# Optimization experiments

Hardware: AMD Instinct MI355X
Metric: run time of the kernel (lower is better)

The kernel has to match this reference:

```python
import jax, jax.numpy as jnp
import numpy as np

S, B, D, H, HD = 2048, 4, 1280, 16, 80  # seq, batch, d_model, heads, head_dim
NSEG = 8


def setup_inputs() -> dict:
    key = jax.random.key(0)
    k0, k1, k2 = jax.random.split(key, 3)
    x = jax.random.normal(k0, (S, B, D), dtype=jnp.float32)
    Wqkv = jax.random.normal(k1, (D, 3 * D), dtype=jnp.float32) * 0.02
    bqkv = jnp.zeros((3 * D,), dtype=jnp.float32)
    Wproj = jax.random.normal(k2, (D, 4 * D), dtype=jnp.float32) * 0.02
    bproj = jnp.zeros((4 * D,), dtype=jnp.float32)
    # 8 equal windows of 256 tokens: [0, 256, 512, ..., 2048]
    cu_seqlens = (jnp.arange(NSEG + 1, dtype=jnp.int32) * (S // NSEG))
    return {"x": x, "Wqkv": Wqkv, "bqkv": bqkv, "Wproj": Wproj,
            "bproj": bproj, "cu_seqlens": cu_seqlens}


def reference(x, Wqkv, bqkv, Wproj, bproj, cu_seqlens):
    s, b, d = x.shape
    qkv = x @ Wqkv + bqkv                     # [s, b, 3d]
    q, k, v = jnp.split(qkv, 3, axis=2)       # each [s, b, d]
    def to_bhsd(t):
        return t.reshape(s, b, H, HD).transpose(1, 2, 0, 3)  # [b, h, s, hd]
    q, k, v = to_bhsd(q), to_bhsd(k), to_bhsd(v)
    # Block-diagonal mask: token t belongs to window searchsorted(cu[1:], t, right)
    pos = jnp.arange(s)
    seg = jnp.searchsorted(cu_seqlens[1:], pos, side='right')  # [s]
    bias = jnp.where(seg[:, None] == seg[None, :], 0.0,
                     jnp.finfo(x.dtype).min)                   # [s, s]
    scale = 1.0 / jnp.sqrt(jnp.asarray(HD, dtype=x.dtype))
    scores = jnp.einsum('bhsd,bhtd->bhst', q, k) * scale + bias
    attn = jax.nn.softmax(scores, axis=-1)
    out = jnp.einsum('bhst,bhtd->bhsd', attn, v)               # [b, h, s, hd]
    context = out.transpose(2, 0, 1, 3).reshape(s, b, H * HD)  # [s, b, d]
    return context @ Wproj + bproj                             # [s, b, 4d]
```

## Files before the change

### kernel.cpp

```cpp
#include <hip/hip_runtime.h>

typedef _Float16 f16;
typedef _Float16 f16x8 __attribute__((ext_vector_type(8)));
typedef _Float16 f16x4 __attribute__((ext_vector_type(4)));
typedef float    f32x4 __attribute__((ext_vector_type(4)));
typedef unsigned int u32t;

#define AS1 __attribute__((address_space(1)))
#define AS3 __attribute__((address_space(3)))

static __device__ __forceinline__ void gload_lds16(const void* g, void* l) {
  __builtin_amdgcn_global_load_lds((const AS1 u32t*)g, (AS3 u32t*)l, 16, 0, 0);
}

static __device__ __forceinline__ f16x8 zero8() {
  f16x8 z;
#pragma unroll
  for (int j = 0; j < 8; ++j) z[j] = (f16)0;
  return z;
}

__global__ void k_cvt_x(const float* __restrict__ in, f16* __restrict__ out, int n4) {
  int stride = gridDim.x * blockDim.x;
  for (int i = blockIdx.x * blockDim.x + threadIdx.x; i < n4; i += stride) {
    float4 v = ((const float4*)in)[i];
    f16x4 o;
    o[0] = (f16)v.x; o[1] = (f16)v.y; o[2] = (f16)v.z; o[3] = (f16)v.w;
    ((f16x4*)out)[i] = o;
  }
}

__global__ void k_cvt_w_t(const float* __restrict__ W, f16* __restrict__ Wt, int N) {
  __shared__ float T[32][33];
  int bk = blockIdx.x % 40;
  int bn = blockIdx.x / 40;
  int k0 = bk * 32, n0 = bn * 32;
  int r = threadIdx.x >> 5;
  int c = threadIdx.x & 31;
#pragma unroll
  for (int i = 0; i < 4; ++i)
    T[r + i * 8][c] = W[(size_t)(k0 + r + i * 8) * N + n0 + c];
  __syncthreads();
#pragma unroll
  for (int i = 0; i < 4; ++i)
    Wt[(size_t)(n0 + r + i * 8) * 1280 + k0 + c] = (f16)T[c][r + i * 8];
}

template<int NCOLS, bool F16OUT>
__global__ __launch_bounds__(256, 2)
void gemm_nt(const f16* __restrict__ A, const f16* __restrict__ Bt,
             const float* __restrict__ bias, void* __restrict__ Cout)
{
  __shared__ __align__(16) char lds[32768];
  f16* const sA = (f16*)lds;
  f16* const sB = (f16*)(lds + 16384);
  const int tid = threadIdx.x;
  const int wave = tid >> 6, lane = tid & 63;
  constexpr int NBN = NCOLS / 128;
  const int bm = blockIdx.x / NBN, bn = blockIdx.x % NBN;
  const long row0 = (long)bm * 128, col0 = (long)bn * 128;

  f32x4 acc[4][4];
#pragma unroll
  for (int i = 0; i < 4; ++i)
#pragma unroll
    for (int j = 0; j < 4; ++j) acc[i][j] = (f32x4){0.f, 0.f, 0.f, 0.f};

  const int wr = (wave >> 1) * 64, wc = (wave & 1) * 64;

  int segr[4], segoff[4];
#pragma unroll
  for (int i = 0; i < 4; ++i) {
    int o = (wave * 4 + i) * 1024 + lane * 16;
    int r = o >> 7, cb = o & 127;
    segr[i] = r;
    segoff[i] = cb ^ ((r & 7) << 4);
  }

  const char* Ab = (const char*)A;
  const char* Bb = (const char*)Bt;

  for (int kt = 0; kt < 20; ++kt) {
    __syncthreads();
#pragma unroll
    for (int i = 0; i < 4; ++i) {
      const char* ga = Ab + ((row0 + segr[i]) * 1280 + kt * 64) * 2 + segoff[i];
      gload_lds16(ga, (char*)sA + (wave * 4 + i) * 1024);
      const char* gb = Bb + ((col0 + segr[i]) * 1280 + kt * 64) * 2 + segoff[i];
      gload_lds16(gb, (char*)sB + (wave * 4 + i) * 1024);
    }
    __syncthreads();

#pragma unroll
    for (int kk = 0; kk < 2; ++kk) {
      const int rl = lane & 15, g = lane >> 4, x7 = lane & 7;
      const int ph = (kk * 4 + g) ^ x7;
      f16x8 af[4], bf[4];
#pragma unroll
      for (int mt = 0; mt < 4; ++mt)
        af[mt] = *(const f16x8*)(sA + (wr + mt * 16 + rl) * 64 + ph * 8);
#pragma unroll
      for (int nt = 0; nt < 4; ++nt)
        bf[nt] = *(const f16x8*)(sB + (wc + nt * 16 + rl) * 64 + ph * 8);
#pragma unroll
      for (int mt = 0; mt < 4; ++mt)
#pragma unroll
        for (int nt = 0; nt < 4; ++nt)
          acc[mt][nt] = __builtin_amdgcn_mfma_f32_16x16x32_f16(af[mt], bf[nt], acc[mt][nt], 0, 0, 0);
    }
  }

  const int rl = lane & 15, g = lane >> 4;
  if (F16OUT) {
    __syncthreads();
    f16* cb = (f16*)lds;
#pragma unroll
    for (int mt = 0; mt < 4; ++mt) {
#pragma unroll
      for (int nt = 0; nt < 4; ++nt) {
        int colc = wc + nt * 16 + rl;
        float bv = bias[col0 + colc];
#pragma unroll
        for (int r = 0; r < 4; ++r) {
          int lrow = wr + mt * 16 + g * 4 + r;
          int phys = (colc >> 3) ^ (lrow & 7);
          cb[lrow * 128 + phys * 8 + (colc & 7)] = (f16)(acc[mt][nt][r] + bv);
        }
      }
    }
    __syncthreads();
    const int row = tid & 127, h = tid >> 7;
    f16* gout = (f16*)Cout + (row0 + row) * NCOLS + col0 + h * 64;
    const f16* src = cb + row * 128;
#pragma unroll
    for (int j = 0; j < 8; ++j) {
      f16x8 v = *(const f16x8*)(src + (((h * 8 + j) ^ (row & 7)) * 8));
      *(f16x8*)(gout + j * 8) = v;
    }
  } else {
#pragma unroll
    for (int mt = 0; mt < 4; ++mt) {
#pragma unroll
      for (int nt = 0; nt < 4; ++nt) {
        long c = col0 + wc + nt * 16 + rl;
        float bv = bias[c];
#pragma unroll
        for (int r = 0; r < 4; ++r) {
          long rr = row0 + wr + mt * 16 + g * 4 + r;
          ((float*)Cout)[rr * NCOLS + c] = acc[mt][nt][r] + bv;
        }
      }
    }
  }
}

__global__ void k_vt(const f16* __restrict__ qkv, f16* __restrict__ vt) {
  __shared__ __align__(16) f16 T[128 * 136];
  int bid = blockIdx.x;
  int sc16 = bid & 15, bh = bid >> 4;
  int b = bh >> 4, h = bh & 15;
  int s0 = sc16 * 128;
  int t = threadIdx.x;
#pragma unroll
  for (int i = 0; i < 5; ++i) {
    int cid = i * 256 + t;
    int s = cid / 10, c = cid % 10;
    const f16* g = qkv + (size_t)((s0 + s) * 4 + b) * 3840 + 2560 + h * 80 + c * 8;
    f16x8 v = *(const f16x8*)g;
    int phys = c ^ ((s >> 3) & 7);
    *(f16x8*)(T + s * 136 + phys * 8) = v;
  }
  __syncthreads();
#pragma unroll
  for (int i = 0; i < 5; ++i) {
    int oid = i * 256 + t;
    int sc8 = oid & 15, hd = oid >> 4;
    f16x8 o;
#pragma unroll
    for (int j = 0; j < 8; ++j) {
      int row = sc8 * 8 + j;
      int phys = (hd >> 3) ^ (sc8 & 7);
      o[j] = T[row * 136 + phys * 8 + (hd & 7)];
    }
    *(f16x8*)(vt + (size_t)(bh * 80 + hd) * 2048 + s0 + sc8 * 8) = o;
  }
}

__global__ __launch_bounds__(512, 2)
void k_attn(const f16* __restrict__ qkv, const f16* __restrict__ vt,
            f16* __restrict__ ctx)
{
  __shared__ __align__(16) f16 sK[256 * 104];
  __shared__ __align__(16) f16 sV[80 * 264];
  __shared__ __align__(16) f16 sP[128 * 72];

  const int bid = blockIdx.x;
  const int qc = bid & 1, seg = (bid >> 1) & 7, h = (bid >> 4) & 15, b = bid >> 8;
  const int t = threadIdx.x;
  const int wave = t >> 6, lane = t & 63;
  const int s_key0 = seg * 256;

#pragma unroll
  for (int i = 0; i < 5; ++i) {
    int cid = i * 512 + t;
    int key = cid / 10, c = cid % 10;
    const f16* g = qkv + (size_t)((s_key0 + key) * 4 + b) * 3840 + 1280 + h * 80 + c * 8;
    *(f16x8*)(sK + key * 104 + c * 8) = *(const f16x8*)g;
  }
  {
    int key = t >> 1, c = t & 1;
    *(f16x8*)(sK + key * 104 + 80 + c * 8) = zero8();
  }
#pragma unroll
  for (int i = 0; i < 5; ++i) {
    int cid = i * 512 + t;
    int hd = cid >> 5, c = cid & 31;
    const f16* g = vt + (size_t)((b * 16 + h) * 80 + hd) * 2048 + s_key0 + c * 8;
    *(f16x8*)(sV + hd * 264 + c * 8) = *(const f16x8*)g;
  }

  const int q0 = s_key0 + qc * 128 + wave * 16;
  const int rl = lane & 15, g = lane >> 4;
  f16x8 qf[3];
  {
    const f16* gq = qkv + (size_t)((q0 + rl) * 4 + b) * 3840 + h * 80;
    qf[0] = *(const f16x8*)(gq + g * 8);
    qf[1] = *(const f16x8*)(gq + 32 + g * 8);
    if (g < 2) qf[2] = *(const f16x8*)(gq + 64 + g * 8);
    else       qf[2] = zero8();
  }
  __syncthreads();

  f32x4 sc[16];
#pragma unroll
  for (int nt = 0; nt < 16; ++nt) sc[nt] = (f32x4){0.f, 0.f, 0.f, 0.f};
#pragma unroll
  for (int nt = 0; nt < 16; ++nt) {
#pragma unroll
    for (int kk = 0; kk < 3; ++kk) {
      f16x8 bf = *(const f16x8*)(sK + (nt * 16 + rl) * 104 + kk * 32 + g * 8);
      sc[nt] = __builtin_amdgcn_mfma_f32_16x16x32_f16(qf[kk], bf, sc[nt], 0, 0, 0);
    }
  }

  const float scale = 0.11180339887498949f;
  float inv[4];
#pragma unroll
  for (int r = 0; r < 4; ++r) {
    float m = -1e30f;
#pragma unroll
    for (int nt = 0; nt < 16; ++nt) m = fmaxf(m, sc[nt][r]);
#pragma unroll
    for (int off = 8; off >= 1; off >>= 1) m = fmaxf(m, __shfl_xor(m, off));
    m *= scale;
    float sum = 0.f;
#pragma unroll
    for (int nt = 0; nt < 16; ++nt) {
      float p = __expf(sc[nt][r] * scale - m);
      sc[nt][r] = p;
      sum += p;
    }
#pragma unroll
    for (int off = 8; off >= 1; off >>= 1) sum += __shfl_xor(sum, off);
    inv[r] = 1.0f / sum;
  }

  f32x4 o[5];
#pragma unroll
  for (int nt = 0; nt < 5; ++nt) o[nt] = (f32x4){0.f, 0.f, 0.f, 0.f};
  const int prow0 = wave * 16;
  for (int ch = 0; ch < 4; ++ch) {
#pragma unroll
    for (int f = 0; f < 4; ++f) {
      int nt = ch * 4 + f;
#pragma unroll
      for (int r = 0; r < 4; ++r)
        sP[(prow0 + g * 4 + r) * 72 + f * 16 + rl] = (f16)sc[nt][r];
    }
#pragma unroll
    for (int kk = 0; kk < 2; ++kk) {
      f16x8 pa = *(const f16x8*)(sP + (prow0 + rl) * 72 + kk * 32 + g * 8);
#pragma unroll
      for (int nt = 0; nt < 5; ++nt) {
        f16x8 vb = *(const f16x8*)(sV + (nt * 16 + rl) * 264 + ch * 64 + kk * 32 + g * 8);
        o[nt] = __builtin_amdgcn_mfma_f32_16x16x32_f16(pa, vb, o[nt], 0, 0, 0);
      }
    }
  }

#pragma unroll
  for (int nt = 0; nt < 5; ++nt) {
    int hd = nt * 16 + rl;
#pragma unroll
    for (int r = 0; r < 4; ++r) {
      long qrow = q0 + g * 4 + r;
      float v = o[nt][r] * inv[r];
      ctx[(qrow * 4 + b) * 1280 + h * 80 + hd] = (f16)v;
    }
  }
}

extern "C" void kernel_launch(void* const* d_in, const int* in_sizes, int n_in,
                              void* d_out, int out_size, void* d_ws, size_t ws_size,
                              hipStream_t stream)
{
  const float* x     = (const float*)d_in[0];
  const float* Wqkv  = (const float*)d_in[1];
  const float* bqkv  = (const float*)d_in[2];
  const float* Wproj = (const float*)d_in[3];
  const float* bproj = (const float*)d_in[4];

  char* ws = (char*)d_ws;
  f16* X16   = (f16*)(ws);
  f16* WQT   = (f16*)(ws + 20971520);
  f16* WPT   = (f16*)(ws + 30801920);
  f16* QKV16 = (f16*)(ws + 43909120);
  f16* VT    = (f16*)(ws + 106823680);
  f16* CTX16 = X16;

  k_cvt_x<<<4096, 256, 0, stream>>>(x, X16, 8192 * 1280 / 4);
  k_cvt_w_t<<<40 * 120, 256, 0, stream>>>(Wqkv, WQT, 3840);
  k_cvt_w_t<<<40 * 160, 256, 0, stream>>>(Wproj, WPT, 5120);
  gemm_nt<3840, true ><<<64 * 30, 256, 0, stream>>>(X16, WQT, bqkv, QKV16);
  k_vt<<<1024, 256, 0, stream>>>(QKV16, VT);
  k_attn<<<1024, 512, 0, stream>>>(QKV16, VT, CTX16);
  gemm_nt<5120, false><<<64 * 40, 256, 0, stream>>>(CTX16, WPT, bproj, d_out);
}
```

Measured before the change: 290.6 us.

## Process whole 256-query window per attention block and split projection GEMM launch

Each attention block now covers a full 256-token window instead of half, with each wave handling two 16-row query tiles that share every K and V fragment load from LDS. This halves the number of blocks and the redundant K/V staging into LDS, at the cost of roughly double the accumulator registers per wave and a larger sP buffer, which may lower occupancy. The output projection GEMM is split into two launches over row halves through a new bm_base parameter, adding one kernel launch.

```diff
diff --git a/kernel.cpp b/kernel.cpp
--- a/kernel.cpp
+++ b/kernel.cpp
@@ -49,7 +49,7 @@
 template<int NCOLS, bool F16OUT>
 __global__ __launch_bounds__(256, 2)
 void gemm_nt(const f16* __restrict__ A, const f16* __restrict__ Bt,
-             const float* __restrict__ bias, void* __restrict__ Cout)
+             const float* __restrict__ bias, void* __restrict__ Cout, int bm_base)
 {
   __shared__ __align__(16) char lds[32768];
   f16* const sA = (f16*)lds;
@@ -57,7 +57,7 @@
   const int tid = threadIdx.x;
   const int wave = tid >> 6, lane = tid & 63;
   constexpr int NBN = NCOLS / 128;
-  const int bm = blockIdx.x / NBN, bn = blockIdx.x % NBN;
+  const int bm = bm_base + blockIdx.x / NBN, bn = blockIdx.x % NBN;
   const long row0 = (long)bm * 128, col0 = (long)bn * 128;
 
   f32x4 acc[4][4];
@@ -192,10 +192,10 @@
 {
   __shared__ __align__(16) f16 sK[256 * 104];
   __shared__ __align__(16) f16 sV[80 * 264];
-  __shared__ __align__(16) f16 sP[128 * 72];
+  __shared__ __align__(16) f16 sP[256 * 72];
 
   const int bid = blockIdx.x;
-  const int qc = bid & 1, seg = (bid >> 1) & 7, h = (bid >> 4) & 15, b = bid >> 8;
+  const int seg = bid & 7, h = (bid >> 3) & 15, b = bid >> 7;
   const int t = threadIdx.x;
   const int wave = t >> 6, lane = t & 63;
   const int s_key0 = seg * 256;
@@ -219,71 +219,80 @@
     *(f16x8*)(sV + hd * 264 + c * 8) = *(const f16x8*)g;
   }
 
-  const int q0 = s_key0 + qc * 128 + wave * 16;
+  const int q0 = s_key0 + wave * 32;
   const int rl = lane & 15, g = lane >> 4;
-  f16x8 qf[3];
+  f16x8 qfl[3], qfh[3];
   {
-    const f16* gq = qkv + (size_t)((q0 + rl) * 4 + b) * 3840 + h * 80;
-    qf[0] = *(const f16x8*)(gq + g * 8);
-    qf[1] = *(const f16x8*)(gq + 32 + g * 8);
-    if (g < 2) qf[2] = *(const f16x8*)(gq + 64 + g * 8);
-    else       qf[2] = zero8();
+    const f16* gl = qkv + (size_t)((q0 + rl) * 4 + b) * 3840 + h * 80;
+    const f16* gh = qkv + (size_t)((q0 + 16 + rl) * 4 + b) * 3840 + h * 80;
+    qfl[0] = *(const f16x8*)(gl + g * 8);
+    qfh[0] = *(const f16x8*)(gh + g * 8);
+    qfl[1] = *(const f16x8*)(gl + 32 + g * 8);
+    qfh[1] = *(const f16x8*)(gh + 32 + g * 8);
+    if (g < 2) { qfl[2] = *(const f16x8*)(gl + 64 + g * 8); qfh[2] = *(const f16x8*)(gh + 64 + g * 8); }
+    else       { qfl[2] = zero8(); qfh[2] = zero8(); }
   }
   __syncthreads();
 
-  f32x4 sc[16];
-#pragma unroll
-  for (int nt = 0; nt < 16; ++nt) sc[nt] = (f32x4){0.f, 0.f, 0.f, 0.f};
+  f32x4 scl[16], sch[16];
+#pragma unroll
+  for (int nt = 0; nt < 16; ++nt) { scl[nt] = (f32x4){0.f,0.f,0.f,0.f}; sch[nt] = (f32x4){0.f,0.f,0.f,0.f}; }
 #pragma unroll
   for (int nt = 0; nt < 16; ++nt) {
 #pragma unroll
     for (int kk = 0; kk < 3; ++kk) {
       f16x8 bf = *(const f16x8*)(sK + (nt * 16 + rl) * 104 + kk * 32 + g * 8);
-      sc[nt] = __builtin_amdgcn_mfma_f32_16x16x32_f16(qf[kk], bf, sc[nt], 0, 0, 0);
+      scl[nt] = __builtin_amdgcn_mfma_f32_16x16x32_f16(qfl[kk], bf, scl[nt], 0, 0, 0);
+      sch[nt] = __builtin_amdgcn_mfma_f32_16x16x32_f16(qfh[kk], bf, sch[nt], 0, 0, 0);
     }
   }
 
   const float scale = 0.11180339887498949f;
-  float inv[4];
+  float invl[4], invh[4];
 #pragma unroll
   for (int r = 0; r < 4; ++r) {
-    float m = -1e30f;
-#pragma unroll
-    for (int nt = 0; nt < 16; ++nt) m = fmaxf(m, sc[nt][r]);
-#pragma unroll
-    for (int off = 8; off >= 1; off >>= 1) m = fmaxf(m, __shfl_xor(m, off));
-    m *= scale;
-    float sum = 0.f;
+    float ml = -1e30f, mh = -1e30f;
+#pragma unroll
+    for (int nt = 0; nt < 16; ++nt) { ml = fmaxf(ml, scl[nt][r]); mh = fmaxf(mh, sch[nt][r]); }
+#pragma unroll
+    for (int off = 8; off >= 1; off >>= 1) { ml = fmaxf(ml, __shfl_xor(ml, off)); mh = fmaxf(mh, __shfl_xor(mh, off)); }
+    ml *= scale; mh *= scale;
+    float suml = 0.f, sumh = 0.f;
 #pragma unroll
     for (int nt = 0; nt < 16; ++nt) {
-      float p = __expf(sc[nt][r] * scale - m);
-      sc[nt][r] = p;
-      sum += p;
-    }
-#pragma unroll
-    for (int off = 8; off >= 1; off >>= 1) sum += __shfl_xor(sum, off);
-    inv[r] = 1.0f / sum;
-  }
-
-  f32x4 o[5];
-#pragma unroll
-  for (int nt = 0; nt < 5; ++nt) o[nt] = (f32x4){0.f, 0.f, 0.f, 0.f};
-  const int prow0 = wave * 16;
+      float pl = __expf(scl[nt][r] * scale - ml);
+      float ph = __expf(sch[nt][r] * scale - mh);
+      scl[nt][r] = pl; sch[nt][r] = ph;
+      suml += pl; sumh += ph;
+    }
+#pragma unroll
+    for (int off = 8; off >= 1; off >>= 1) { suml += __shfl_xor(suml, off); sumh += __shfl_xor(sumh, off); }
+    invl[r] = 1.0f / suml; invh[r] = 1.0f / sumh;
+  }
+
+  f32x4 ol[5], oh[5];
+#pragma unroll
+  for (int nt = 0; nt < 5; ++nt) { ol[nt] = (f32x4){0.f,0.f,0.f,0.f}; oh[nt] = (f32x4){0.f,0.f,0.f,0.f}; }
+  const int prow0 = wave * 32;
   for (int ch = 0; ch < 4; ++ch) {
 #pragma unroll
     for (int f = 0; f < 4; ++f) {
       int nt = ch * 4 + f;
 #pragma unroll
-      for (int r = 0; r < 4; ++r)
-        sP[(prow0 + g * 4 + r) * 72 + f * 16 + rl] = (f16)sc[nt][r];
+      for (int r = 0; r < 4; ++r) {
+        sP[(prow0 + g * 4 + r) * 72 + f * 16 + rl]      = (f16)scl[nt][r];
+        sP[(prow0 + 16 + g * 4 + r) * 72 + f * 16 + rl] = (f16)sch[nt][r];
+      }
     }
 #pragma unroll
     for (int kk = 0; kk < 2; ++kk) {
-      f16x8 pa = *(const f16x8*)(sP + (prow0 + rl) * 72 + kk * 32 + g * 8);
+      f16x8 pal = *(const f16x8*)(sP + (prow0 + rl) * 72 + kk * 32 + g * 8);
+      f16x8 pah = *(const f16x8*)(sP + (prow0 + 16 + rl) * 72 + kk * 32 + g * 8);
 #pragma unroll
       for (int nt = 0; nt < 5; ++nt) {
         f16x8 vb = *(const f16x8*)(sV + (nt * 16 + rl) * 264 + ch * 64 + kk * 32 + g * 8);
-        o[nt] = __builtin_amdgcn_mfma_f32_16x16x32_f16(pa, vb, o[nt], 0, 0, 0);
+        ol[nt] = __builtin_amdgcn_mfma_f32_16x16x32_f16(pal, vb, ol[nt], 0, 0, 0);
+        oh[nt] = __builtin_amdgcn_mfma_f32_16x16x32_f16(pah, vb, oh[nt], 0, 0, 0);
       }
     }
   }
@@ -293,9 +302,10 @@
     int hd = nt * 16 + rl;
 #pragma unroll
     for (int r = 0; r < 4; ++r) {
-      long qrow = q0 + g * 4 + r;
-      float v = o[nt][r] * inv[r];
-      ctx[(qrow * 4 + b) * 1280 + h * 80 + hd] = (f16)v;
+      long qrl = q0 + g * 4 + r;
+      ctx[(qrl * 4 + b) * 1280 + h * 80 + hd] = (f16)(ol[nt][r] * invl[r]);
+      long qrh = q0 + 16 + g * 4 + r;
+      ctx[(qrh * 4 + b) * 1280 + h * 80 + hd] = (f16)(oh[nt][r] * invh[r]);
     }
   }
 }
@@ -321,8 +331,9 @@
   k_cvt_x<<<4096, 256, 0, stream>>>(x, X16, 8192 * 1280 / 4);
   k_cvt_w_t<<<40 * 120, 256, 0, stream>>>(Wqkv, WQT, 3840);
   k_cvt_w_t<<<40 * 160, 256, 0, stream>>>(Wproj, WPT, 5120);
-  gemm_nt<3840, true ><<<64 * 30, 256, 0, stream>>>(X16, WQT, bqkv, QKV16);
+  gemm_nt<3840, true ><<<64 * 30, 256, 0, stream>>>(X16, WQT, bqkv, QKV16, 0);
   k_vt<<<1024, 256, 0, stream>>>(QKV16, VT);
-  k_attn<<<1024, 512, 0, stream>>>(QKV16, VT, CTX16);
-  gemm_nt<5120, false><<<64 * 40, 256, 0, stream>>>(CTX16, WPT, bproj, d_out);
-}
+  k_attn<<<512, 512, 0, stream>>>(QKV16, VT, CTX16);
+  gemm_nt<5120, false><<<32 * 40, 256, 0, stream>>>(CTX16, WPT, bproj, d_out, 0);
+  gemm_nt<5120, false><<<32 * 40, 256, 0, stream>>>(CTX16, WPT, bproj, d_out, 32);
+}
```

Result: no change. 295.3 us (+1.6%).
